# Kernel optimization log

Hardware: AMD Instinct MI355X
Metric: run time of the kernel (lower is better)

Reference implementation:

```python
import jax, jax.numpy as jnp
import numpy as np

NUM_EXPERTS = 64
NUM_SELECTED = 2
HASH_BITS = 32


def setup_inputs() -> dict:
    key = jax.random.key(0)
    k1, k2 = jax.random.split(key)
    hidden_states = jax.random.normal(k1, (4, 4096, 2048), dtype=jnp.float32)
    # torch Linear weight [out_features, in_features], init normal(std=0.01), bias zeros
    hash_w = jax.random.normal(k2, (NUM_SELECTED * HASH_BITS, 2048), dtype=jnp.float32) * 0.01
    hash_b = jnp.zeros((NUM_SELECTED * HASH_BITS,), dtype=jnp.float32)
    return {"hidden_states": hidden_states, "hash_w": hash_w, "hash_b": hash_b}


def reference(hidden_states, hash_w, hash_b):
    B, S, H = hidden_states.shape
    T = B * S
    x = hidden_states.reshape(T, H)
    # hash projection: [T, k*32]
    h = x @ hash_w.T + hash_b
    bits = (h > 0).astype(jnp.int32).reshape(T, NUM_SELECTED, HASH_BITS)
    cand = bits.sum(axis=-1) % NUM_EXPERTS  # [T, k] candidate expert per slot

    # Sequential dedup (vectorized over tokens): for each slot i in order, if the
    # candidate collides with an already-chosen expert for that token, advance
    # (e+1) % E until a free expert is found (always exists since k <= E).
    used = jnp.zeros((T, NUM_EXPERTS), dtype=bool)
    offs = jnp.arange(NUM_EXPERTS)
    chosen = []
    for i in range(NUM_SELECTED):
        e = cand[:, i]  # [T]
        pos = (e[:, None] + offs[None, :]) % NUM_EXPERTS  # [T, E] probe sequence
        probed = jnp.take_along_axis(used, pos, axis=1)  # [T, E] used flags along probe
        off = jnp.argmax(~probed, axis=1)  # first free offset (0 if candidate free)
        ne = (e + off) % NUM_EXPERTS
        used = used | jax.nn.one_hot(ne, NUM_EXPERTS, dtype=bool)
        chosen.append(ne)
    expert_indices = jnp.stack(chosen, axis=1).astype(jnp.int32)  # [T, k]
    expert_weights = jnp.full((T, NUM_SELECTED), 1.0 / NUM_SELECTED, dtype=jnp.float32)
    router_logits = jnp.zeros((T, NUM_EXPERTS), dtype=jnp.float32)
    return expert_weights, expert_indices, router_logits
```

## Files before the change

kernel.cpp:

```cpp
#include <hip/hip_runtime.h>


constexpr int H_DIM  = 2048;
constexpr int NJ     = 64;
constexpr int TOKB   = 16;
constexpr int KW     = 512;
constexpr int KSTEPS = KW / 32;

typedef __attribute__((ext_vector_type(8))) short  bf16x8;
typedef __attribute__((ext_vector_type(4))) float  f32x4;

__device__ __forceinline__ unsigned int bf16rne(float f) {
    unsigned int u = __float_as_uint(f);
    return (u + 0x7FFFu + ((u >> 16) & 1u)) >> 16;
}

__device__ __forceinline__ void split8(const f32x4 a0, const f32x4 a1,
                                       bf16x8& hi, bf16x8& lo) {
    union { bf16x8 v; unsigned int u[4]; } H, L;
    const unsigned int u0 = __float_as_uint(a0.x), u1 = __float_as_uint(a0.y);
    const unsigned int u2 = __float_as_uint(a0.z), u3 = __float_as_uint(a0.w);
    const unsigned int u4 = __float_as_uint(a1.x), u5 = __float_as_uint(a1.y);
    const unsigned int u6 = __float_as_uint(a1.z), u7 = __float_as_uint(a1.w);
    H.u[0] = (u0 >> 16) | (u1 & 0xFFFF0000u);
    H.u[1] = (u2 >> 16) | (u3 & 0xFFFF0000u);
    H.u[2] = (u4 >> 16) | (u5 & 0xFFFF0000u);
    H.u[3] = (u6 >> 16) | (u7 & 0xFFFF0000u);
    const float l0 = a0.x - __uint_as_float(u0 & 0xFFFF0000u);
    const float l1 = a0.y - __uint_as_float(u1 & 0xFFFF0000u);
    const float l2 = a0.z - __uint_as_float(u2 & 0xFFFF0000u);
    const float l3 = a0.w - __uint_as_float(u3 & 0xFFFF0000u);
    const float l4 = a1.x - __uint_as_float(u4 & 0xFFFF0000u);
    const float l5 = a1.y - __uint_as_float(u5 & 0xFFFF0000u);
    const float l6 = a1.z - __uint_as_float(u6 & 0xFFFF0000u);
    const float l7 = a1.w - __uint_as_float(u7 & 0xFFFF0000u);
    L.u[0] = bf16rne(l0) | (bf16rne(l1) << 16);
    L.u[1] = bf16rne(l2) | (bf16rne(l3) << 16);
    L.u[2] = bf16rne(l4) | (bf16rne(l5) << 16);
    L.u[3] = bf16rne(l6) | (bf16rne(l7) << 16);
    hi = H.v; lo = L.v;
}

__global__ __launch_bounds__(256, 2) void hash_mfma_kernel(
    const float* __restrict__ x,
    const float* __restrict__ w,
    const float* __restrict__ b,
    float* __restrict__ out,
    int T)
{
    __shared__ float red[3 * 64 * 16];

    const int tid  = threadIdx.x;
    const int wv   = tid >> 6;
    const int lane = tid & 63;
    const int row  = lane & 15;
    const int kq   = lane >> 4;
    const int tokB = blockIdx.x * TOKB;

    const float* xA = x + (size_t)(tokB + row) * H_DIM + wv * KW + kq * 8;
    const float* wB = w + (size_t)row * H_DIM + wv * KW + kq * 8;

    f32x4 acc[4];
#pragma unroll
    for (int jt = 0; jt < 4; ++jt) acc[jt] = (f32x4){0.f, 0.f, 0.f, 0.f};

#pragma unroll 2
    for (int ks = 0; ks < KSTEPS; ++ks) {
        const int k0 = ks * 32;
        bf16x8 AH, AL;
        {
            const f32x4 a0 = *(const f32x4*)(xA + k0);
            const f32x4 a1 = *(const f32x4*)(xA + k0 + 4);
            split8(a0, a1, AH, AL);
        }
#pragma unroll
        for (int jt = 0; jt < 4; ++jt) {
            const float* wp = wB + (size_t)jt * 16 * H_DIM + k0;
            const f32x4 b0 = *(const f32x4*)(wp);
            const f32x4 b1 = *(const f32x4*)(wp + 4);
            bf16x8 BH, BL;
            split8(b0, b1, BH, BL);
            acc[jt] = __builtin_amdgcn_mfma_f32_16x16x32_bf16(AL, BH, acc[jt], 0, 0, 0);
            acc[jt] = __builtin_amdgcn_mfma_f32_16x16x32_bf16(AH, BL, acc[jt], 0, 0, 0);
            acc[jt] = __builtin_amdgcn_mfma_f32_16x16x32_bf16(AH, BH, acc[jt], 0, 0, 0);
        }
    }

    if (wv) {
        float* rp = red + ((wv - 1) * 64 + lane) * 16;
#pragma unroll
        for (int jt = 0; jt < 4; ++jt) *(f32x4*)(rp + jt * 4) = acc[jt];
    }
    __syncthreads();

    if (wv == 0) {
#pragma unroll
        for (int w2 = 0; w2 < 3; ++w2)
#pragma unroll
            for (int jt = 0; jt < 4; ++jt) {
                const f32x4 t = *(const f32x4*)(red + (w2 * 64 + lane) * 16 + jt * 4);
                acc[jt].x += t.x; acc[jt].y += t.y; acc[jt].z += t.z; acc[jt].w += t.w;
            }

        float bias[4];
#pragma unroll
        for (int jt = 0; jt < 4; ++jt) bias[jt] = b[jt * 16 + row];

        const float TH = 5e-5f;
        int c0 = 0, c1 = 0;
        const int myg = (lane >> 2) & 3;
        const int myr = lane & 3;
#pragma unroll
        for (int jt = 0; jt < 4; ++jt)
#pragma unroll
            for (int r = 0; r < 4; ++r) {
                const float h = acc[jt][r] + bias[jt];
                bool pos;
                if (__builtin_expect(fabsf(h) < TH, 0)) {
                    const float* xr = x + (size_t)(tokB + (lane >> 4) * 4 + r) * H_DIM;
                    const float* wr = w + (size_t)(jt * 16 + row) * H_DIM;
                    double sd = (double)bias[jt];
                    for (int k = 0; k < H_DIM; ++k)
                        sd += (double)xr[k] * (double)wr[k];
                    pos = (sd > 0.0);
                } else {
                    pos = (h > 0.0f);
                }
                const unsigned long long bal = __ballot(pos);
                const int add = ((myr == r) ? 1 : 0) *
                    __popc((unsigned int)((bal >> (myg * 16)) & 0xFFFFu));
                if (jt < 2) c0 += add; else c1 += add;
            }

        if (lane < TOKB) {
            const int t  = tokB + lane;
            const int i1 = c1 + ((c1 == c0) ? 1 : 0);
            float2 wq; wq.x = 0.5f; wq.y = 0.5f;
            *(float2*)(out + 2 * (size_t)t) = wq;
            float2 iq; iq.x = (float)c0; iq.y = (float)i1;
            *(float2*)(out + 2 * (size_t)T + 2 * (size_t)t) = iq;
        }
    }

    f32x4 z = (f32x4){0.f, 0.f, 0.f, 0.f};
    *(f32x4*)(out + 4 * (size_t)T + (size_t)tokB * NJ + (size_t)tid * 4) = z;
}

extern "C" void kernel_launch(void* const* d_in, const int* in_sizes, int n_in,
                              void* d_out, int out_size, void* d_ws, size_t ws_size,
                              hipStream_t stream) {
    const float* x = (const float*)d_in[0];
    const float* w = (const float*)d_in[1];
    const float* b = (const float*)d_in[2];
    float* out = (float*)d_out;
    const int T = in_sizes[0] / H_DIM;
    hash_mfma_kernel<<<dim3(T / TOKB), dim3(256), 0, stream>>>(x, w, b, out, T);
}
```

Measured before the change: 313.4 us.

## Software-pipeline global loads with inline asm and manual vmcnt waits

Replaces the K loop with a fully unrolled, double-buffered pipeline. Raw `global_load_dwordx4` inline asm prefetches the next step's weight tiles and the activation tile two steps ahead, and explicit `s_waitcnt vmcnt` gates each step. The goal is to hide global memory latency behind the split-bf16 MFMA work, which the plain loop exposed. The cost is more live vector registers and a fragile hand-counted waitcnt scheme that the compiler cannot check; it also uses 32-bit byte offsets.

```diff
diff --git a/kernel.cpp b/kernel.cpp
--- a/kernel.cpp
+++ b/kernel.cpp
@@ -9,6 +9,9 @@
 
 typedef __attribute__((ext_vector_type(8))) short  bf16x8;
 typedef __attribute__((ext_vector_type(4))) float  f32x4;
+
+struct raw8  { f32x4 lo, hi; };
+struct bquad { raw8 b0, b1, b2, b3; };
 
 __device__ __forceinline__ unsigned int bf16rne(float f) {
     unsigned int u = __float_as_uint(f);
@@ -41,6 +44,36 @@
     hi = H.v; lo = L.v;
 }
 
+#define GLOAD(dst, BASE, VOFF, IMM) \
+    asm volatile("global_load_dwordx4 %0, %1, %2 offset:%c3" \
+                 : "=v"(dst) : "v"(VOFF), "s"(BASE), "n"(IMM))
+
+#define ISSUE_A(AR, kk) do { \
+    GLOAD(AR.lo, x, voffA, (kk) * 128);      \
+    GLOAD(AR.hi, x, voffA, (kk) * 128 + 16); } while (0)
+
+#define ISSUE_B(BQ, kk) do { \
+    GLOAD(BQ.b0.lo, w, voffB0, (kk) * 128); GLOAD(BQ.b0.hi, w, voffB0, (kk) * 128 + 16); \
+    GLOAD(BQ.b1.lo, w, voffB1, (kk) * 128); GLOAD(BQ.b1.hi, w, voffB1, (kk) * 128 + 16); \
+    GLOAD(BQ.b2.lo, w, voffB2, (kk) * 128); GLOAD(BQ.b2.hi, w, voffB2, (kk) * 128 + 16); \
+    GLOAD(BQ.b3.lo, w, voffB3, (kk) * 128); GLOAD(BQ.b3.hi, w, voffB3, (kk) * 128 + 16); } while (0)
+
+#define JT_STEP(jt, BRV) { \
+    bf16x8 BH, BL; split8(BRV.lo, BRV.hi, BH, BL); \
+    acc[jt] = __builtin_amdgcn_mfma_f32_16x16x32_bf16(AL, BH, acc[jt], 0, 0, 0); \
+    acc[jt] = __builtin_amdgcn_mfma_f32_16x16x32_bf16(AH, BL, acc[jt], 0, 0, 0); \
+    acc[jt] = __builtin_amdgcn_mfma_f32_16x16x32_bf16(AH, BH, acc[jt], 0, 0, 0); }
+
+#define STEP(ks, AR, BC, BN) do { \
+    if ((ks) < KSTEPS - 1) asm volatile("s_waitcnt vmcnt(2)" ::: "memory"); \
+    else                   asm volatile("s_waitcnt vmcnt(0)" ::: "memory"); \
+    __builtin_amdgcn_sched_barrier(0); \
+    bf16x8 AH, AL; split8(AR.lo, AR.hi, AH, AL); \
+    if ((ks) + 1 < KSTEPS) { ISSUE_B(BN, (ks) + 1); } \
+    if ((ks) + 2 < KSTEPS) { ISSUE_A(AR, (ks) + 2); } \
+    JT_STEP(0, BC.b0); JT_STEP(1, BC.b1); JT_STEP(2, BC.b2); JT_STEP(3, BC.b3); \
+} while (0)
+
 __global__ __launch_bounds__(256, 2) void hash_mfma_kernel(
     const float* __restrict__ x,
     const float* __restrict__ w,
@@ -57,34 +90,31 @@
     const int kq   = lane >> 4;
     const int tokB = blockIdx.x * TOKB;
 
-    const float* xA = x + (size_t)(tokB + row) * H_DIM + wv * KW + kq * 8;
-    const float* wB = w + (size_t)row * H_DIM + wv * KW + kq * 8;
+    const unsigned int voffA  = (((unsigned)(tokB + row) * H_DIM) + wv * KW + kq * 8) * 4u;
+    const unsigned int voffB0 = (((unsigned)(0 * 16 + row) * H_DIM) + wv * KW + kq * 8) * 4u;
+    const unsigned int voffB1 = voffB0 + 16u * H_DIM * 4u;
+    const unsigned int voffB2 = voffB0 + 32u * H_DIM * 4u;
+    const unsigned int voffB3 = voffB0 + 48u * H_DIM * 4u;
 
     f32x4 acc[4];
 #pragma unroll
     for (int jt = 0; jt < 4; ++jt) acc[jt] = (f32x4){0.f, 0.f, 0.f, 0.f};
 
-#pragma unroll 2
-    for (int ks = 0; ks < KSTEPS; ++ks) {
-        const int k0 = ks * 32;
-        bf16x8 AH, AL;
-        {
-            const f32x4 a0 = *(const f32x4*)(xA + k0);
-            const f32x4 a1 = *(const f32x4*)(xA + k0 + 4);
-            split8(a0, a1, AH, AL);
-        }
-#pragma unroll
-        for (int jt = 0; jt < 4; ++jt) {
-            const float* wp = wB + (size_t)jt * 16 * H_DIM + k0;
-            const f32x4 b0 = *(const f32x4*)(wp);
-            const f32x4 b1 = *(const f32x4*)(wp + 4);
-            bf16x8 BH, BL;
-            split8(b0, b1, BH, BL);
-            acc[jt] = __builtin_amdgcn_mfma_f32_16x16x32_bf16(AL, BH, acc[jt], 0, 0, 0);
-            acc[jt] = __builtin_amdgcn_mfma_f32_16x16x32_bf16(AH, BL, acc[jt], 0, 0, 0);
-            acc[jt] = __builtin_amdgcn_mfma_f32_16x16x32_bf16(AH, BH, acc[jt], 0, 0, 0);
-        }
-    }
+    raw8  arE, arO;
+    bquad brE, brO;
+
+    ISSUE_B(brE, 0);
+    ISSUE_A(arE, 0);
+    ISSUE_A(arO, 1);
+
+    STEP( 0, arE, brE, brO);  STEP( 1, arO, brO, brE);
+    STEP( 2, arE, brE, brO);  STEP( 3, arO, brO, brE);
+    STEP( 4, arE, brE, brO);  STEP( 5, arO, brO, brE);
+    STEP( 6, arE, brE, brO);  STEP( 7, arO, brO, brE);
+    STEP( 8, arE, brE, brO);  STEP( 9, arO, brO, brE);
+    STEP(10, arE, brE, brO);  STEP(11, arO, brO, brE);
+    STEP(12, arE, brE, brO);  STEP(13, arO, brO, brE);
+    STEP(14, arE, brE, brO);  STEP(15, arO, brO, brE);
 
     if (wv) {
         float* rp = red + ((wv - 1) * 64 + lane) * 16;
```

After: 297.2 us. 5.2% less time.
